# Performance work log

Measured on AMD Instinct MI355X. Metric: run time of the kernel, lower is better.

## Reference

```python
import jax, jax.numpy as jnp
import numpy as np

NUM_NEG_INDICES_FOR_LOSS = 5
NUM_NEG_PAIRS = 64
C, H, W = 256, 512, 512


def setup_inputs() -> dict:
    key = jax.random.key(0)
    k1, k2, k3 = jax.random.split(key, 3)
    feats1 = jax.random.normal(k1, (1, C, H, W), dtype=jnp.float32)
    feats2 = jax.random.normal(k2, (1, C, H, W), dtype=jnp.float32)
    positive_pairs = jax.random.randint(k3, (1, NUM_NEG_PAIRS, 2), 0, H * W, dtype=jnp.int64)
    return {"feats1": feats1, "feats2": feats2, "positive_pairs": positive_pairs}


def reference(feats1, feats2, positive_pairs):
    # feats*: [1, C, H, W]; positive_pairs: [1, P, 2] with P == NUM_NEG_PAIRS
    b, c, h, w = feats1.shape
    f1 = feats1.reshape(c, -1)  # [C, HW] (valid because b == 1, matching torch view)
    f2 = feats2.reshape(c, -1)  # [C, HW]
    idx = positive_pairs[0, :, 0]  # [P] anchor pixel indices into flattened image 1
    sel = f1[:, idx].T             # [P, C] anchor descriptors
    # Squared L2 distance from each anchor to every pixel of image 2 via the
    # ||a||^2 + ||b||^2 - 2 a.b expansion (one [P,C]x[C,HW] GEMM).
    d = (jnp.sum(sel * sel, axis=1, keepdims=True)
         + jnp.sum(f2 * f2, axis=0)[None, :]
         - 2.0 * (sel @ f2))       # [P, HW]
    d = jax.nn.relu(d)             # matches functional.relu (also clamps fp error)
    # Hardest negatives = smallest distances. NOTE: the torch neighborhood-mask
    # exclusion compares a float distance VALUE against an int index array, so
    # it is dead code in practice -> effective math is plain top-k smallest.
    neg_vals, _ = jax.lax.top_k(-d, NUM_NEG_INDICES_FOR_LOSS)  # [P, 5]
    per_pair = jnp.mean(-neg_vals, axis=1)                     # [P]
    return jnp.sum(per_pair) / NUM_NEG_PAIRS
```

## Files before the change

kernel.cpp:

```cpp
#include <hip/hip_runtime.h>
#include <hip/hip_bf16.h>

#define HW_   262144
#define C_    256
#define NP_   64
#define BCOLS 128
#define NBLK_ 2048
#define SENT  3.0e38f

typedef __attribute__((ext_vector_type(8))) __bf16 bf16x8;
typedef __attribute__((ext_vector_type(4))) float f32x4;

__device__ __forceinline__ void top5_insert(float (&t)[5], float v) {
  if (v < t[4]) {
    t[4] = v;
    if (t[4] < t[3]) { float x = t[3]; t[3] = t[4]; t[4] = x; }
    if (t[3] < t[2]) { float x = t[2]; t[2] = t[3]; t[3] = x; }
    if (t[2] < t[1]) { float x = t[1]; t[1] = t[2]; t[2] = x; }
    if (t[1] < t[0]) { float x = t[0]; t[0] = t[1]; t[1] = x; }
  }
}

__global__ void gather_sel_kernel(const float* __restrict__ f1,
                                  const void* __restrict__ pairs,
                                  unsigned short* __restrict__ selb,
                                  float* __restrict__ n_p) {
  __shared__ float red[256];
  __shared__ int sidx;
  const int p = blockIdx.x, t = threadIdx.x;
  if (t == 0) {
    const long long* ll = (const long long*)pairs;
    const int* ii = (const int*)pairs;
    bool is64 = true;
    for (int k = 0; k < 8; ++k) {
      long long v = ll[k];
      if (v < 0 || v >= (long long)HW_) is64 = false;
    }
    sidx = is64 ? (int)ll[2 * p] : ii[2 * p];
  }
  __syncthreads();
  const int idx = sidx;
  float v = f1[(size_t)t * HW_ + idx];
  __bf16 b = (__bf16)v;
  selb[p * 256 + t] = __builtin_bit_cast(unsigned short, b);
  red[t] = v * v;
  __syncthreads();
  for (int s = 128; s > 0; s >>= 1) {
    if (t < s) red[t] += red[t + s];
    __syncthreads();
  }
  if (t == 0) n_p[p] = red[0];
}

__global__ __launch_bounds__(256, 3) void dist_topk_kernel(
    const float* __restrict__ f2, const unsigned short* __restrict__ selb,
    const float* __restrict__ n_p, float* __restrict__ cand) {
  __shared__ __align__(16) char smemB[49152];
  float* smemF = (float*)smemB;
  const int tid = threadIdx.x;
  const int w = tid >> 6, lane = tid & 63;
  const int m_l = lane & 15, kq = lane >> 4;
  const int j0 = blockIdx.x * BCOLS;
  const int ch_row = tid >> 5;
  const int ch_c4 = (tid & 31) * 4;

  {
    const uint4* src = (const uint4*)selb;
#pragma unroll
    for (int i = 0; i < 8; ++i) {
      const int idx = i * 256 + tid;
      const int m = idx >> 5;
      unsigned off = (unsigned)(idx * 16) ^ ((m & 7) << 4);
      *(uint4*)(smemB + off) = src[idx];
    }
  }

#define STAGE_LOAD(R, T)                                                        \
  _Pragma("unroll") for (int i = 0; i < 4; ++i) {                               \
    const int row = i * 8 + ch_row;                                             \
    R[i] = *(const float4*)(f2 + (size_t)((T) * 32 + row) * HW_ + j0 + ch_c4);  \
  }
#define STAGE_WRITE(R, BUF)                                                     \
  _Pragma("unroll") for (int i = 0; i < 4; ++i) {                               \
    const int row = i * 8 + ch_row;                                             \
    ushort4 pk;                                                                 \
    pk.x = __builtin_bit_cast(unsigned short, (__bf16)R[i].x);                  \
    pk.y = __builtin_bit_cast(unsigned short, (__bf16)R[i].y);                  \
    pk.z = __builtin_bit_cast(unsigned short, (__bf16)R[i].z);                  \
    pk.w = __builtin_bit_cast(unsigned short, (__bf16)R[i].w);                  \
    *(ushort4*)(smemB + 32768 + (BUF) * 8192 + row * 256 + ch_c4 * 2) = pk;     \
  }

  {
    float4 r[4];
    STAGE_LOAD(r, 0)
    STAGE_WRITE(r, 0)
  }
  __syncthreads();

  f32x4 acc[4][2];
#pragma unroll
  for (int mt = 0; mt < 4; ++mt)
#pragma unroll
    for (int nt = 0; nt < 2; ++nt) acc[mt][nt] = (f32x4){0.f, 0.f, 0.f, 0.f};
  float njp[2] = {0.f, 0.f};

#pragma unroll 1
  for (int t = 0; t < 8; ++t) {
    float4 r[4];
    if (t < 7) { STAGE_LOAD(r, t + 1) }

    const char* Bb = smemB + 32768 + (t & 1) * 8192;
    bf16x8 afr[4];
#pragma unroll
    for (int mt = 0; mt < 4; ++mt) {
      unsigned offA =
          (unsigned)((mt * 16 + m_l) * 512 + kq * 16 + t * 64) ^ ((m_l & 7) << 4);
      afr[mt] = *(const bf16x8*)(smemB + offA);
    }
    bf16x8 bfr[2];
#pragma unroll
    for (int nt = 0; nt < 2; ++nt) {
      const int col = w * 32 + nt * 16 + m_l;
#pragma unroll
      for (int e = 0; e < 8; ++e) {
        unsigned short us =
            *(const unsigned short*)(Bb + (kq * 8 + e) * 256 + col * 2);
        bfr[nt][e] = __builtin_bit_cast(__bf16, us);
        float fv = __builtin_bit_cast(float, (unsigned)us << 16);
        njp[nt] = fmaf(fv, fv, njp[nt]);
      }
    }
#pragma unroll
    for (int mt = 0; mt < 4; ++mt)
#pragma unroll
      for (int nt = 0; nt < 2; ++nt)
        acc[mt][nt] = __builtin_amdgcn_mfma_f32_16x16x32_bf16(
            afr[mt], bfr[nt], acc[mt][nt], 0, 0, 0);

    if (t < 7) { STAGE_WRITE(r, (t + 1) & 1) }
    __syncthreads();
  }
#undef STAGE_LOAD
#undef STAGE_WRITE

  float njc[2];
#pragma unroll
  for (int nt = 0; nt < 2; ++nt) {
    float v = njp[nt];
    v += __shfl_xor(v, 16);
    v += __shfl_xor(v, 32);
    njc[nt] = v;
  }

#pragma unroll
  for (int mt = 0; mt < 4; ++mt) {
#pragma unroll
    for (int r = 0; r < 4; ++r) {
      const int pair = mt * 16 + kq * 4 + r;
      const float np = n_p[pair];
#pragma unroll
      for (int nt = 0; nt < 2; ++nt) {
        const int col = w * 32 + nt * 16 + m_l;
        float d = np + njc[nt] - 2.0f * acc[mt][nt][r];
        smemF[pair * 128 + (col ^ (pair & 31))] = fmaxf(d, 0.0f);
      }
    }
  }
  __syncthreads();

  const int pp = tid & 63, q = tid >> 6;
  float t5[5] = {SENT, SENT, SENT, SENT, SENT};
#pragma unroll 4
  for (int i = 0; i < 32; ++i) {
    const int col = q * 32 + i;
    float v = smemF[pp * 128 + (col ^ (pp & 31))];
    top5_insert(t5, v);
  }
  __syncthreads();
#pragma unroll
  for (int k = 0; k < 5; ++k) smemF[tid * 5 + k] = t5[k];
  __syncthreads();
  if (tid < 64) {
    float m5[5] = {SENT, SENT, SENT, SENT, SENT};
    for (int g = 0; g < 4; ++g)
#pragma unroll
      for (int k = 0; k < 5; ++k) top5_insert(m5, smemF[(g * 64 + tid) * 5 + k]);
    float* cc = cand + (size_t)blockIdx.x * (NP_ * 5) + tid * 5;
#pragma unroll
    for (int k = 0; k < 5; ++k) cc[k] = m5[k];
  }
}

__global__ void topk_reduce_kernel(const float* __restrict__ cand,
                                   float* __restrict__ mean5) {
  __shared__ float lds[256 * 5];
  const int p = blockIdx.x, tid = threadIdx.x;
  float t5[5] = {SENT, SENT, SENT, SENT, SENT};
  for (int b = tid; b < NBLK_; b += 256) {
    const float* cc = cand + (size_t)b * (NP_ * 5) + p * 5;
#pragma unroll
    for (int k = 0; k < 5; ++k) top5_insert(t5, cc[k]);
  }
#pragma unroll
  for (int k = 0; k < 5; ++k) lds[tid * 5 + k] = t5[k];
  __syncthreads();
  float m2[5] = {SENT, SENT, SENT, SENT, SENT};
  if (tid < 32) {
    for (int t2 = tid * 8; t2 < tid * 8 + 8; ++t2)
#pragma unroll
      for (int k = 0; k < 5; ++k) top5_insert(m2, lds[t2 * 5 + k]);
  }
  __syncthreads();
  if (tid < 32) {
#pragma unroll
    for (int k = 0; k < 5; ++k) lds[tid * 5 + k] = m2[k];
  }
  __syncthreads();
  if (tid == 0) {
    float f[5] = {SENT, SENT, SENT, SENT, SENT};
    for (int t2 = 0; t2 < 32; ++t2)
#pragma unroll
      for (int k = 0; k < 5; ++k) top5_insert(f, lds[t2 * 5 + k]);
    mean5[p] = (f[0] + f[1] + f[2] + f[3] + f[4]) * 0.2f;
  }
}

__global__ void final_sum_kernel(const float* __restrict__ mean5,
                                 float* __restrict__ out) {
  const int tid = threadIdx.x;
  float v = mean5[tid];
  for (int off = 32; off > 0; off >>= 1) v += __shfl_down(v, off);
  if (tid == 0) out[0] = v * (1.0f / 64.0f);
}

extern "C" void kernel_launch(void* const* d_in, const int* in_sizes, int n_in,
                              void* d_out, int out_size, void* d_ws, size_t ws_size,
                              hipStream_t stream) {
  const float* f1 = (const float*)d_in[0];
  const float* f2 = (const float*)d_in[1];
  const void* pairs = d_in[2];
  float* out = (float*)d_out;
  float* ws = (float*)d_ws;

  float*          n_p   = ws;
  unsigned short* selb  = (unsigned short*)(ws + 64);
  float*          cand  = ws + 64 + 8192;
  float*          mean5 = ws + 64 + 8192 + 655360;

  gather_sel_kernel<<<NP_, 256, 0, stream>>>(f1, pairs, selb, n_p);
  dist_topk_kernel<<<NBLK_, 256, 0, stream>>>(f2, selb, n_p, cand);
  topk_reduce_kernel<<<NP_, 256, 0, stream>>>(cand, mean5);
  final_sum_kernel<<<1, 64, 0, stream>>>(mean5, out);
}
```

Measured before the change: 93.78 us.

## Widen dist tiles to 256 columns with 512 threads and two-stage register prefetch

```diff
diff --git a/kernel.cpp b/kernel.cpp
--- a/kernel.cpp
+++ b/kernel.cpp
@@ -4,8 +4,7 @@
 #define HW_   262144
 #define C_    256
 #define NP_   64
-#define BCOLS 128
-#define NBLK_ 2048
+#define NBLK_ 1024
 #define SENT  3.0e38f
 
 typedef __attribute__((ext_vector_type(8))) __bf16 bf16x8;
@@ -52,51 +51,52 @@
   if (t == 0) n_p[p] = red[0];
 }
 
-__global__ __launch_bounds__(256, 3) void dist_topk_kernel(
+__global__ __launch_bounds__(512, 4) void dist_topk_kernel(
     const float* __restrict__ f2, const unsigned short* __restrict__ selb,
     const float* __restrict__ n_p, float* __restrict__ cand) {
-  __shared__ __align__(16) char smemB[49152];
+  __shared__ __align__(16) char smemB[65536];
   float* smemF = (float*)smemB;
   const int tid = threadIdx.x;
   const int w = tid >> 6, lane = tid & 63;
   const int m_l = lane & 15, kq = lane >> 4;
-  const int j0 = blockIdx.x * BCOLS;
-  const int ch_row = tid >> 5;
-  const int ch_c4 = (tid & 31) * 4;
+  const int j0 = blockIdx.x * 256;
+
+  float4 rA[4], rB[4];
+#define LOADT(R, T)                                                            \
+  _Pragma("unroll") for (int i = 0; i < 4; ++i) {                              \
+    R[i] = *(const float4*)(f2 + (size_t)((T) * 32 + i * 8 + w) * HW_ + j0 +   \
+                            (lane << 2));                                      \
+  }
+#define WRITET(R, BUF)                                                         \
+  _Pragma("unroll") for (int i = 0; i < 4; ++i) {                              \
+    const int r = i * 8 + w;                                                   \
+    const unsigned Xr = (unsigned)(((r & 7) << 4) ^ ((r >> 3) << 5));          \
+    ushort4 pk;                                                                \
+    pk.x = __builtin_bit_cast(unsigned short, (__bf16)R[i].x);                 \
+    pk.y = __builtin_bit_cast(unsigned short, (__bf16)R[i].y);                 \
+    pk.z = __builtin_bit_cast(unsigned short, (__bf16)R[i].z);                 \
+    pk.w = __builtin_bit_cast(unsigned short, (__bf16)R[i].w);                 \
+    *(ushort4*)(smemB + 32768 + (BUF) * 16384 + r * 512 +                      \
+                (((unsigned)(lane << 3)) ^ Xr)) = pk;                          \
+  }
+
+  LOADT(rA, 0)
+  LOADT(rB, 1)
 
   {
     const uint4* src = (const uint4*)selb;
 #pragma unroll
-    for (int i = 0; i < 8; ++i) {
-      const int idx = i * 256 + tid;
+    for (int i = 0; i < 4; ++i) {
+      const int idx = i * 512 + tid;
       const int m = idx >> 5;
       unsigned off = (unsigned)(idx * 16) ^ ((m & 7) << 4);
       *(uint4*)(smemB + off) = src[idx];
     }
   }
-
-#define STAGE_LOAD(R, T)                                                        \
-  _Pragma("unroll") for (int i = 0; i < 4; ++i) {                               \
-    const int row = i * 8 + ch_row;                                             \
-    R[i] = *(const float4*)(f2 + (size_t)((T) * 32 + row) * HW_ + j0 + ch_c4);  \
-  }
-#define STAGE_WRITE(R, BUF)                                                     \
-  _Pragma("unroll") for (int i = 0; i < 4; ++i) {                               \
-    const int row = i * 8 + ch_row;                                             \
-    ushort4 pk;                                                                 \
-    pk.x = __builtin_bit_cast(unsigned short, (__bf16)R[i].x);                  \
-    pk.y = __builtin_bit_cast(unsigned short, (__bf16)R[i].y);                  \
-    pk.z = __builtin_bit_cast(unsigned short, (__bf16)R[i].z);                  \
-    pk.w = __builtin_bit_cast(unsigned short, (__bf16)R[i].w);                  \
-    *(ushort4*)(smemB + 32768 + (BUF) * 8192 + row * 256 + ch_c4 * 2) = pk;     \
-  }
-
-  {
-    float4 r[4];
-    STAGE_LOAD(r, 0)
-    STAGE_WRITE(r, 0)
-  }
-  __syncthreads();
+  WRITET(rA, 0)
+  asm volatile("s_waitcnt lgkmcnt(0)" ::: "memory");
+  __builtin_amdgcn_sched_barrier(0);
+  __builtin_amdgcn_s_barrier();
 
   f32x4 acc[4][2];
 #pragma unroll
@@ -105,44 +105,54 @@
     for (int nt = 0; nt < 2; ++nt) acc[mt][nt] = (f32x4){0.f, 0.f, 0.f, 0.f};
   float njp[2] = {0.f, 0.f};
 
-#pragma unroll 1
+  const unsigned colx2_0 = ((unsigned)((w * 32 + m_l) * 2)) ^ ((unsigned)kq << 5);
+  const unsigned colx2_1 = colx2_0 ^ 32u;
+  const unsigned kqrow = (unsigned)kq * 4096;
+
+#pragma unroll
   for (int t = 0; t < 8; ++t) {
-    float4 r[4];
-    if (t < 7) { STAGE_LOAD(r, t + 1) }
-
-    const char* Bb = smemB + 32768 + (t & 1) * 8192;
-    bf16x8 afr[4];
-#pragma unroll
-    for (int mt = 0; mt < 4; ++mt) {
-      unsigned offA =
-          (unsigned)((mt * 16 + m_l) * 512 + kq * 16 + t * 64) ^ ((m_l & 7) << 4);
-      afr[mt] = *(const bf16x8*)(smemB + offA);
-    }
-    bf16x8 bfr[2];
-#pragma unroll
-    for (int nt = 0; nt < 2; ++nt) {
-      const int col = w * 32 + nt * 16 + m_l;
-#pragma unroll
-      for (int e = 0; e < 8; ++e) {
-        unsigned short us =
-            *(const unsigned short*)(Bb + (kq * 8 + e) * 256 + col * 2);
-        bfr[nt][e] = __builtin_bit_cast(__bf16, us);
-        float fv = __builtin_bit_cast(float, (unsigned)us << 16);
-        njp[nt] = fmaf(fv, fv, njp[nt]);
+    if (t < 6) {
+      if ((t & 1) == 0) { LOADT(rA, t + 2) } else { LOADT(rB, t + 2) }
+    }
+    {
+      const char* Bb = smemB + 32768 + (t & 1) * 16384 + kqrow;
+      bf16x8 afr[4];
+#pragma unroll
+      for (int mt = 0; mt < 4; ++mt) {
+        unsigned offA =
+            (unsigned)((mt * 16 + m_l) * 512 + kq * 16 + t * 64) ^
+            ((m_l & 7) << 4);
+        afr[mt] = *(const bf16x8*)(smemB + offA);
       }
-    }
-#pragma unroll
-    for (int mt = 0; mt < 4; ++mt)
-#pragma unroll
-      for (int nt = 0; nt < 2; ++nt)
-        acc[mt][nt] = __builtin_amdgcn_mfma_f32_16x16x32_bf16(
-            afr[mt], bfr[nt], acc[mt][nt], 0, 0, 0);
-
-    if (t < 7) { STAGE_WRITE(r, (t + 1) & 1) }
-    __syncthreads();
-  }
-#undef STAGE_LOAD
-#undef STAGE_WRITE
+      bf16x8 bfr[2];
+#pragma unroll
+      for (int nt = 0; nt < 2; ++nt) {
+        const unsigned cx = nt ? colx2_1 : colx2_0;
+#pragma unroll
+        for (int e = 0; e < 8; ++e) {
+          unsigned short us =
+              *(const unsigned short*)(Bb + e * 512 + (cx ^ (e << 4)));
+          bfr[nt][e] = __builtin_bit_cast(__bf16, us);
+          float fv = __builtin_bit_cast(float, (unsigned)us << 16);
+          njp[nt] = fmaf(fv, fv, njp[nt]);
+        }
+      }
+#pragma unroll
+      for (int mt = 0; mt < 4; ++mt)
+#pragma unroll
+        for (int nt = 0; nt < 2; ++nt)
+          acc[mt][nt] = __builtin_amdgcn_mfma_f32_16x16x32_bf16(
+              afr[mt], bfr[nt], acc[mt][nt], 0, 0, 0);
+    }
+    if (t < 7) {
+      if (t & 1) { WRITET(rA, 0) } else { WRITET(rB, 1) }
+      asm volatile("s_waitcnt lgkmcnt(0)" ::: "memory");
+      __builtin_amdgcn_sched_barrier(0);
+      __builtin_amdgcn_s_barrier();
+    }
+  }
+#undef LOADT
+#undef WRITET
 
   float njc[2];
 #pragma unroll
@@ -153,6 +163,8 @@
     njc[nt] = v;
   }
 
+  __syncthreads();
+
 #pragma unroll
   for (int mt = 0; mt < 4; ++mt) {
 #pragma unroll
@@ -163,7 +175,7 @@
       for (int nt = 0; nt < 2; ++nt) {
         const int col = w * 32 + nt * 16 + m_l;
         float d = np + njc[nt] - 2.0f * acc[mt][nt][r];
-        smemF[pair * 128 + (col ^ (pair & 31))] = fmaxf(d, 0.0f);
+        smemF[pair * 256 + (col ^ (pair & 31))] = fmaxf(d, 0.0f);
       }
     }
   }
@@ -174,7 +186,7 @@
 #pragma unroll 4
   for (int i = 0; i < 32; ++i) {
     const int col = q * 32 + i;
-    float v = smemF[pp * 128 + (col ^ (pp & 31))];
+    float v = smemF[pp * 256 + (col ^ (pp & 31))];
     top5_insert(t5, v);
   }
   __syncthreads();
@@ -183,7 +195,7 @@
   __syncthreads();
   if (tid < 64) {
     float m5[5] = {SENT, SENT, SENT, SENT, SENT};
-    for (int g = 0; g < 4; ++g)
+    for (int g = 0; g < 8; ++g)
 #pragma unroll
       for (int k = 0; k < 5; ++k) top5_insert(m5, smemF[(g * 64 + tid) * 5 + k]);
     float* cc = cand + (size_t)blockIdx.x * (NP_ * 5) + tid * 5;
@@ -246,10 +258,10 @@
   float*          n_p   = ws;
   unsigned short* selb  = (unsigned short*)(ws + 64);
   float*          cand  = ws + 64 + 8192;
-  float*          mean5 = ws + 64 + 8192 + 655360;
+  float*          mean5 = ws + 64 + 8192 + 327680;
 
   gather_sel_kernel<<<NP_, 256, 0, stream>>>(f1, pairs, selb, n_p);
-  dist_topk_kernel<<<NBLK_, 256, 0, stream>>>(f2, selb, n_p, cand);
+  dist_topk_kernel<<<NBLK_, 512, 0, stream>>>(f2, selb, n_p, cand);
   topk_reduce_kernel<<<NP_, 256, 0, stream>>>(cand, mean5);
   final_sum_kernel<<<1, 64, 0, stream>>>(mean5, out);
 }
```

After: 83.13 us. -11.4%, faster.
